# Optimization experiments

Hardware: AMD Instinct MI355X
Metric: run time of the kernel (lower is better)

Reference implementation:

```python
import jax, jax.numpy as jnp
import numpy as np

N_ITERS = 3
EPS = 1e-5


def _ln(x, g, b):
    mu = jnp.mean(x, axis=-1, keepdims=True)
    var = jnp.mean((x - mu) ** 2, axis=-1, keepdims=True)
    return (x - mu) * jax.lax.rsqrt(var + EPS) * g + b


def setup_inputs() -> dict:
    key = jax.random.key(0)
    ks = iter(jax.random.split(key, 32))
    B, N, D_in, H, K = 128, 1024, 192, 128, 3

    def lin(o, i):
        w = (jax.random.normal(next(ks), (o, i)) / np.sqrt(i)).astype(jnp.float32)
        return w, jnp.zeros((o,), jnp.float32)

    Wp, bp = lin(H, D_in)
    Wq, bq = lin(H, H)
    Wk, bk = lin(H, H)
    Wv, bv = lin(H, H)
    Wih, bih = lin(3 * H, H)   # GRUCell input weights, stacked [r, z, n]
    Whh, bhh = lin(3 * H, H)   # GRUCell hidden weights
    W1, b1 = lin(2 * H, H)     # MLP expand
    W2, b2 = lin(H, 2 * H)     # MLP project
    ones = jnp.ones((H,), jnp.float32)
    zeros = jnp.zeros((H,), jnp.float32)

    return {
        "patch_tokens": jax.random.normal(next(ks), (B, N, D_in), jnp.float32),
        "noise": jax.random.normal(next(ks), (B, K, H), jnp.float32),
        "slot_mu": (jax.random.normal(next(ks), (1, K, H)) * 0.02).astype(jnp.float32),
        "slot_log_sigma": jnp.zeros((1, K, H), jnp.float32),
        "Wp": Wp, "bp": bp, "g_in": ones, "b_in": zeros,
        "Wq": Wq, "bq": bq, "Wk": Wk, "bk": bk, "Wv": Wv, "bv": bv,
        "Wih": Wih, "bih": bih, "Whh": Whh, "bhh": bhh,
        "g_s": ones, "b_s": zeros,
        "W1": W1, "b1": b1, "W2": W2, "b2": b2,
        "g_m": ones, "b_m": zeros,
    }


def reference(patch_tokens, noise, slot_mu, slot_log_sigma,
              Wp, bp, g_in, b_in,
              Wq, bq, Wk, bk, Wv, bv,
              Wih, bih, Whh, bhh,
              g_s, b_s, W1, b1, W2, b2, g_m, b_m):
    H = slot_mu.shape[-1]
    scale = 1.0 / jnp.sqrt(jnp.asarray(H, patch_tokens.dtype))

    # project + LayerNorm inputs once (k, v depend only on inputs -> hoisted)
    inputs = _ln(patch_tokens @ Wp.T + bp, g_in, b_in)      # (B, N, H)
    k = inputs @ Wk.T + bk                                  # (B, N, H)
    v = inputs @ Wv.T + bv                                  # (B, N, H)

    slots = slot_mu + jnp.exp(slot_log_sigma) * noise       # (B, K, H)

    def gru_cell(x, h):
        gi = x @ Wih.T + bih                                # (B, K, 3H)
        gh = h @ Whh.T + bhh
        ir, iz, inn = jnp.split(gi, 3, axis=-1)
        hr, hz, hn = jnp.split(gh, 3, axis=-1)
        r = jax.nn.sigmoid(ir + hr)
        z = jax.nn.sigmoid(iz + hz)
        n = jnp.tanh(inn + r * hn)
        return (1.0 - z) * n + z * h

    attn_weights = None
    for _ in range(N_ITERS):
        slots_prev = slots
        s = _ln(slots, g_s, b_s)
        q = s @ Wq.T + bq                                   # (B, K, H)
        attn = jnp.einsum('bkd,bnd->bkn', q, k) * scale     # (B, K, N)
        attn_weights = jax.nn.softmax(attn, axis=1)         # softmax over slots
        updates = jnp.einsum('bkn,bnd->bkd', attn_weights, v)
        slots = gru_cell(updates, slots_prev)
        h = _ln(slots, g_m, b_m)
        slots = slots + (jax.nn.gelu(h @ W1.T + b1, approximate=False) @ W2.T + b2)

    return slots, attn_weights
```

## Files before the change

kernel.cpp:

```cpp
#include <hip/hip_runtime.h>
#include <math.h>

constexpr float EPS = 1e-5f;
constexpr float SCALE = 0.08838834764831845f;

using f32x4  = __attribute__((ext_vector_type(4))) float;
using bf16x8 = __attribute__((ext_vector_type(8))) short;
using us8    = __attribute__((ext_vector_type(8))) unsigned short;

__device__ __forceinline__ unsigned short f2b_rne(float f) {
    unsigned int x = __float_as_uint(f);
    return (unsigned short)((x + 0x7fffu + ((x >> 16) & 1u)) >> 16);
}

__device__ __forceinline__ int swz32(int row, int k8) {
    int f = (row & 3) ^ ((row >> 2) & 3);
    return row * 32 + ((k8 ^ f) << 3);
}

__global__ __launch_bounds__(256) void split_weights_kernel(
    const float* __restrict__ Wp, const float* __restrict__ Wk,
    const float* __restrict__ Wv, unsigned short* __restrict__ hi,
    unsigned short* __restrict__ lo)
{
    int idx = blockIdx.x * 256 + threadIdx.x;
    float v;
    if (idx < 24576)      v = Wp[idx];
    else if (idx < 40960) v = Wk[idx - 24576];
    else                  v = Wv[idx - 40960];
    unsigned int bits = __float_as_uint(v);
    hi[idx] = (unsigned short)(bits >> 16);
    lo[idx] = f2b_rne(v - __uint_as_float(bits & 0xffff0000u));
}

__global__ __launch_bounds__(256) void pack_weights_kernel(
    const float* __restrict__ Wih, const float* __restrict__ Whh,
    const float* __restrict__ W1, const float* __restrict__ W2,
    const float* __restrict__ Wq, float4* __restrict__ out)
{
    int idx = blockIdx.x * 256 + threadIdx.x;
    const float* src; int OUT, base, K;
    if (idx < 12288)      { src = Wih; OUT = 384; base = 0;     K = 128; }
    else if (idx < 24576) { src = Whh; OUT = 384; base = 12288; K = 128; }
    else if (idx < 32768) { src = W1;  OUT = 256; base = 24576; K = 128; }
    else if (idx < 40960) { src = W2;  OUT = 128; base = 32768; K = 256; }
    else                  { src = Wq;  OUT = 128; base = 40960; K = 128; }
    int li = idx - base;
    int kq = li / OUT, t = li - kq * OUT;
    float4 v;
    v.x = src[(size_t)t * K + 4 * kq];
    v.y = src[(size_t)t * K + 4 * kq + 1];
    v.z = src[(size_t)t * K + 4 * kq + 2];
    v.w = src[(size_t)t * K + 4 * kq + 3];
    out[idx] = v;
}

__global__ __launch_bounds__(256, 3) void fused_proj_kv_kernel(
    const float* __restrict__ patch,
    const unsigned short* __restrict__ Wphi, const unsigned short* __restrict__ Wplo,
    const unsigned short* __restrict__ Wkhi, const unsigned short* __restrict__ Wklo,
    const unsigned short* __restrict__ Wvhi, const unsigned short* __restrict__ Wvlo,
    const float* __restrict__ biasp, const float* __restrict__ g_in,
    const float* __restrict__ b_in, const float* __restrict__ biask,
    const float* __restrict__ biasv,
    float* __restrict__ kout, float* __restrict__ vout)
{
    __shared__ __align__(16) unsigned short mem[24576];

    const int tid  = threadIdx.x;
    const int lane = tid & 63, wave = tid >> 6;
    const int ln15 = lane & 15, quad = lane >> 4;
    const int m0   = blockIdx.x * 64;

    const int wrow = wave * 16;
    f32x4 acc1[8];
#pragma unroll
    for (int nt = 0; nt < 8; nt++)
#pragma unroll
        for (int r = 0; r < 4; r++) acc1[nt][r] = 0.f;

    const int arow = tid >> 2, ak8 = tid & 3;
    const float* aptr = patch + (size_t)(m0 + arow) * 192 + ak8 * 8;
    float4 pa0 = *(const float4*)aptr;
    float4 pa1 = *(const float4*)(aptr + 4);
    us8 pbh[2], pbl[2];
    int boff[2];
#pragma unroll
    for (int i = 0; i < 2; i++) {
        int c = tid + 256 * i;
        boff[i] = (c >> 2) * 192 + (c & 3) * 8;
        pbh[i] = *(const us8*)(Wphi + boff[i]);
        pbl[i] = *(const us8*)(Wplo + boff[i]);
    }

    const int ea = swz32(wrow + ln15, quad);

    for (int kk = 0; kk < 192; kk += 32) {
        {
            float va[8] = {pa0.x, pa0.y, pa0.z, pa0.w, pa1.x, pa1.y, pa1.z, pa1.w};
            us8 h, l;
#pragma unroll
            for (int j = 0; j < 8; j++) {
                unsigned int bits = __float_as_uint(va[j]);
                h[j] = (unsigned short)(bits >> 16);
                l[j] = f2b_rne(va[j] - __uint_as_float(bits & 0xffff0000u));
            }
            int e = swz32(arow, ak8);
            *(us8*)&mem[e]        = h;
            *(us8*)&mem[2048 + e] = l;
        }
#pragma unroll
        for (int i = 0; i < 2; i++) {
            int c = tid + 256 * i;
            int e = swz32(c >> 2, c & 3);
            *(us8*)&mem[4096 + e] = pbh[i];
            *(us8*)&mem[8192 + e] = pbl[i];
        }
        __syncthreads();

        int kn = kk + 32;
        if (kn < 192) {
            pa0 = *(const float4*)(aptr + kn);
            pa1 = *(const float4*)(aptr + kn + 4);
#pragma unroll
            for (int i = 0; i < 2; i++) {
                pbh[i] = *(const us8*)(Wphi + boff[i] + kn);
                pbl[i] = *(const us8*)(Wplo + boff[i] + kn);
            }
        }

        bf16x8 ah = *(const bf16x8*)&mem[ea];
        bf16x8 al = *(const bf16x8*)&mem[2048 + ea];
#pragma unroll
        for (int nt = 0; nt < 8; nt++) {
            int eb = swz32(nt * 16 + ln15, quad);
            bf16x8 bh = *(const bf16x8*)&mem[4096 + eb];
            bf16x8 bl = *(const bf16x8*)&mem[8192 + eb];
            acc1[nt] = __builtin_amdgcn_mfma_f32_16x16x32_bf16(ah, bh, acc1[nt], 0, 0, 0);
            acc1[nt] = __builtin_amdgcn_mfma_f32_16x16x32_bf16(ah, bl, acc1[nt], 0, 0, 0);
            acc1[nt] = __builtin_amdgcn_mfma_f32_16x16x32_bf16(al, bh, acc1[nt], 0, 0, 0);
        }
        __syncthreads();
    }

    us8 pw[4];
#pragma unroll
    for (int i = 0; i < 4; i++) {
        const unsigned short* pl = (i >> 1) ? Wklo : Wkhi;
        int c = tid + (i & 1) * 256;
        pw[i] = *(const us8*)(pl + (size_t)(c >> 2) * 128 + (c & 3) * 8);
    }

    {
        float bb[8], gg[8], be[8];
#pragma unroll
        for (int nt = 0; nt < 8; nt++) {
            int col = nt * 16 + ln15;
            bb[nt] = biasp[col]; gg[nt] = g_in[col]; be[nt] = b_in[col];
        }
#pragma unroll
        for (int nt = 0; nt < 8; nt++)
#pragma unroll
            for (int r = 0; r < 4; r++) acc1[nt][r] += bb[nt];

        float mu[4], rs[4];
#pragma unroll
        for (int r = 0; r < 4; r++) {
            float s = 0.f, s2 = 0.f;
#pragma unroll
            for (int nt = 0; nt < 8; nt++) {
                float v = acc1[nt][r];
                s += v; s2 += v * v;
            }
#pragma unroll
            for (int off = 1; off < 16; off <<= 1) {
                s  += __shfl_xor(s,  off, 64);
                s2 += __shfl_xor(s2, off, 64);
            }
            float m = s * (1.f / 128.f);
            mu[r] = m;
            rs[r] = rsqrtf(s2 * (1.f / 128.f) - m * m + EPS);
        }
#pragma unroll
        for (int nt = 0; nt < 8; nt++)
#pragma unroll
            for (int r = 0; r < 4; r++) {
                float v = (acc1[nt][r] - mu[r]) * rs[r] * gg[nt] + be[nt];
                int row = wrow + quad * 4 + r, col = nt * 16 + ln15;
                int xi = (row * 128 + col) ^ ((row & 7) << 3);
                unsigned int bits = __float_as_uint(v);
                mem[xi]        = (unsigned short)(bits >> 16);
                mem[8192 + xi] = f2b_rne(v - __uint_as_float(bits & 0xffff0000u));
            }
    }

    const int R  = (wave & 1) * 32;
    const int Cb = (wave >> 1) * 64;
    const int xorx = (ln15 & 7) << 3;

    float bbk[4], bbv[4];
#pragma unroll
    for (int nt = 0; nt < 4; nt++) {
        int col = Cb + nt * 16 + ln15;
        bbk[nt] = biask[col];
        bbv[nt] = biasv[col];
    }

    f32x4 acc[2][4];
#pragma unroll
    for (int mt = 0; mt < 2; mt++)
#pragma unroll
        for (int nt = 0; nt < 4; nt++)
#pragma unroll
            for (int r = 0; r < 4; r++) acc[mt][nt][r] = 0.f;

    for (int s = 0; s < 8; s++) {
#pragma unroll
        for (int i = 0; i < 4; i++) {
            int c = tid + (i & 1) * 256;
            int e = 16384 + (i >> 1) * 4096 + swz32(c >> 2, c & 3);
            *(us8*)&mem[e] = pw[i];
        }
        __syncthreads();

        if (s < 7) {
            int sn = s + 1, kkn = (sn & 3) * 32;
            const unsigned short* ph = (sn >> 2) ? Wvhi : Wkhi;
            const unsigned short* po = (sn >> 2) ? Wvlo : Wklo;
#pragma unroll
            for (int i = 0; i < 4; i++) {
                const unsigned short* pl = (i >> 1) ? po : ph;
                int c = tid + (i & 1) * 256;
                pw[i] = *(const us8*)(pl + (size_t)(c >> 2) * 128 + (c & 3) * 8 + kkn);
            }
        }

        int kk = (s & 3) * 32;
        bf16x8 xh[2], xl[2];
#pragma unroll
        for (int mt = 0; mt < 2; mt++) {
            int row = R + mt * 16 + ln15;
            int ei = (row * 128 + kk + quad * 8) ^ xorx;
            xh[mt] = *(const bf16x8*)&mem[ei];
            xl[mt] = *(const bf16x8*)&mem[8192 + ei];
        }
#pragma unroll
        for (int nt = 0; nt < 4; nt++) {
            int eb = 16384 + swz32(Cb + nt * 16 + ln15, quad);
            bf16x8 wh = *(const bf16x8*)&mem[eb];
            bf16x8 wl = *(const bf16x8*)&mem[4096 + eb];
#pragma unroll
            for (int mt = 0; mt < 2; mt++) {
                acc[mt][nt] = __builtin_amdgcn_mfma_f32_16x16x32_bf16(xh[mt], wh, acc[mt][nt], 0, 0, 0);
                acc[mt][nt] = __builtin_amdgcn_mfma_f32_16x16x32_bf16(xh[mt], wl, acc[mt][nt], 0, 0, 0);
                acc[mt][nt] = __builtin_amdgcn_mfma_f32_16x16x32_bf16(xl[mt], wh, acc[mt][nt], 0, 0, 0);
            }
        }

        if (s == 3) {
#pragma unroll
            for (int mt = 0; mt < 2; mt++)
#pragma unroll
                for (int nt = 0; nt < 4; nt++)
#pragma unroll
                    for (int r = 0; r < 4; r++) {
                        size_t o = (size_t)(m0 + R + mt * 16 + quad * 4 + r) * 128
                                 + Cb + nt * 16 + ln15;
                        kout[o] = acc[mt][nt][r] + bbk[nt];
                        acc[mt][nt][r] = 0.f;
                    }
        }
        if (s < 7) __syncthreads();
    }

#pragma unroll
    for (int mt = 0; mt < 2; mt++)
#pragma unroll
        for (int nt = 0; nt < 4; nt++)
#pragma unroll
            for (int r = 0; r < 4; r++) {
                size_t o = (size_t)(m0 + R + mt * 16 + quad * 4 + r) * 128
                         + Cb + nt * 16 + ln15;
                vout[o] = acc[mt][nt][r] + bbv[nt];
            }
}

__global__ __launch_bounds__(128) void init_lnq_kernel(
    const float* __restrict__ noise, const float* __restrict__ smu,
    const float* __restrict__ sls, const float* __restrict__ g_s,
    const float* __restrict__ b_s, const float4* __restrict__ WqT4,
    const float* __restrict__ bq, float* __restrict__ slots,
    float* __restrict__ q)
{
    __shared__ float s_l[128];
    __shared__ float red[4];
    const int row = blockIdx.x, tid = threadIdx.x;
    const int k = row % 3;
    float x = smu[k * 128 + tid] + expf(sls[k * 128 + tid]) * noise[row * 128 + tid];
    slots[row * 128 + tid] = x;

    float s = x, s2 = x * x;
#pragma unroll
    for (int off = 32; off >= 1; off >>= 1) {
        s += __shfl_down(s, off, 64); s2 += __shfl_down(s2, off, 64);
    }
    if ((tid & 63) == 0) { red[tid >> 6] = s; red[2 + (tid >> 6)] = s2; }
    __syncthreads();
    float S = red[0] + red[1], S2 = red[2] + red[3];
    float m = S * (1.f / 128.f);
    float r = rsqrtf(S2 * (1.f / 128.f) - m * m + EPS);
    s_l[tid] = (x - m) * r * g_s[tid] + b_s[tid];
    __syncthreads();

    float a = bq[tid];
#pragma unroll 8
    for (int kq = 0; kq < 32; kq++) {
        float4 w = WqT4[kq * 128 + tid];
        a += s_l[4 * kq] * w.x + s_l[4 * kq + 1] * w.y
           + s_l[4 * kq + 2] * w.z + s_l[4 * kq + 3] * w.w;
    }
    q[row * 128 + tid] = a;
}

__global__ __launch_bounds__(256) void attn_kernel(
    const float* __restrict__ q, const float* __restrict__ kbuf,
    const float* __restrict__ vbuf, float* __restrict__ upd_part,
    float* __restrict__ attn_out, int write_attn)
{
    __shared__ float q_l[3][132];
    __shared__ __align__(16) float kv[64][132];
    __shared__ float lg[3][64];
    __shared__ float w_l[3][64];
    const int b = blockIdx.y, chunk = blockIdx.x, n0 = chunk * 64, tid = threadIdx.x;

    for (int idx = tid; idx < 384; idx += 256) {
        int s = idx >> 7, c = idx & 127;
        q_l[s][c + (c >> 5)] = q[b * 384 + idx];
    }
    const float4* vg = (const float4*)(vbuf + ((size_t)b * 1024 + n0) * 128);
    for (int idx = tid; idx < 2048; idx += 256) {
        int n = idx >> 5, c = (idx & 31) * 4;
        *(float4*)&kv[n][c] = vg[idx];
    }
    const int n = tid >> 2, q4 = tid & 3;
    float4 kr[8];
    const float4* kg4 = (const float4*)(kbuf + ((size_t)b * 1024 + n0 + n) * 128 + q4 * 32);
#pragma unroll
    for (int i = 0; i < 8; i++) kr[i] = kg4[i];
    __syncthreads();

    {
        const float* q0 = &q_l[0][q4 * 33];
        const float* q1 = &q_l[1][q4 * 33];
        const float* q2 = &q_l[2][q4 * 33];
        float p0 = 0.f, p1 = 0.f, p2 = 0.f;
#pragma unroll
        for (int i = 0; i < 8; i++) {
            float kx[4] = {kr[i].x, kr[i].y, kr[i].z, kr[i].w};
#pragma unroll
            for (int j = 0; j < 4; j++) {
                float vv = kx[j];
                p0 += q0[4 * i + j] * vv;
                p1 += q1[4 * i + j] * vv;
                p2 += q2[4 * i + j] * vv;
            }
        }
        p0 += __shfl_xor(p0, 1, 64); p0 += __shfl_xor(p0, 2, 64);
        p1 += __shfl_xor(p1, 1, 64); p1 += __shfl_xor(p1, 2, 64);
        p2 += __shfl_xor(p2, 1, 64); p2 += __shfl_xor(p2, 2, 64);
        if (q4 == 0) {
            lg[0][n] = p0 * SCALE; lg[1][n] = p1 * SCALE; lg[2][n] = p2 * SCALE;
        }
    }
    __syncthreads();

    if (tid < 64) {
        float l0 = lg[0][tid], l1 = lg[1][tid], l2 = lg[2][tid];
        float m = fmaxf(l0, fmaxf(l1, l2));
        float e0 = expf(l0 - m), e1 = expf(l1 - m), e2 = expf(l2 - m);
        float inv = 1.f / (e0 + e1 + e2);
        w_l[0][tid] = e0 * inv; w_l[1][tid] = e1 * inv; w_l[2][tid] = e2 * inv;
        if (write_attn) {
            attn_out[b * 3072 + n0 + tid]        = e0 * inv;
            attn_out[b * 3072 + 1024 + n0 + tid] = e1 * inv;
            attn_out[b * 3072 + 2048 + n0 + tid] = e2 * inv;
        }
    }
    __syncthreads();

    if (tid < 128) {
        float p0 = 0.f, p1 = 0.f, p2 = 0.f;
#pragma unroll 8
        for (int nn = 0; nn < 64; nn++) {
            float vv = kv[nn][tid];
            p0 += w_l[0][nn] * vv; p1 += w_l[1][nn] * vv; p2 += w_l[2][nn] * vv;
        }
        size_t base = (((size_t)b * 16 + chunk) * 3) * 128 + tid;
        upd_part[base]       = p0;
        upd_part[base + 128] = p1;
        upd_part[base + 256] = p2;
    }
}

__global__ __launch_bounds__(384) void gru_mlp_kernel(
    const float* __restrict__ slots_in, const float* __restrict__ upd_part,
    const float4* __restrict__ WihT4, const float* __restrict__ bih,
    const float4* __restrict__ WhhT4, const float* __restrict__ bhh,
    const float* __restrict__ g_m, const float* __restrict__ b_m,
    const float4* __restrict__ W1T4, const float* __restrict__ b1,
    const float4* __restrict__ W2T4, const float* __restrict__ b2,
    const float* __restrict__ g_s, const float* __restrict__ b_s,
    const float4* __restrict__ WqT4, const float* __restrict__ bq,
    float* __restrict__ slots_out, float* __restrict__ q_out, int write_q)
{
    __shared__ float u2[2][128];
    __shared__ float u_l[128], h_l[128];
    __shared__ float r_l[128], z_l[128], in_l[128], hn_l[128];
    __shared__ float n_l[128], hid_l[256], w2p[256];
    __shared__ float red[4];
    const int row = blockIdx.x, tid = threadIdx.x;
    const int bb_ = row / 3, ss = row - bb_ * 3;

    if (tid < 256) {
        int col = tid & 127, half = tid >> 7;
        const float* up = upd_part + (((size_t)bb_ * 16 + half * 8) * 3 + ss) * 128 + col;
        float u = 0.f;
#pragma unroll
        for (int c = 0; c < 8; c++) u += up[(size_t)c * 384];
        u2[half][col] = u;
        if (half == 0) h_l[col] = slots_in[row * 128 + col];
    }
    __syncthreads();
    if (tid < 128) u_l[tid] = u2[0][tid] + u2[1][tid];
    __syncthreads();

    {
        float gi = bih[tid], gh = bhh[tid];
#pragma unroll 8
        for (int kq = 0; kq < 32; kq++) {
            float4 a = WihT4[kq * 384 + tid];
            float4 c = WhhT4[kq * 384 + tid];
            gi += u_l[4 * kq] * a.x + u_l[4 * kq + 1] * a.y
                + u_l[4 * kq + 2] * a.z + u_l[4 * kq + 3] * a.w;
            gh += h_l[4 * kq] * c.x + h_l[4 * kq + 1] * c.y
                + h_l[4 * kq + 2] * c.z + h_l[4 * kq + 3] * c.w;
        }
        if (tid < 128)      r_l[tid] = 1.f / (1.f + expf(-(gi + gh)));
        else if (tid < 256) z_l[tid - 128] = 1.f / (1.f + expf(-(gi + gh)));
        else { in_l[tid - 256] = gi; hn_l[tid - 256] = gh; }
    }
    __syncthreads();

    float hnew = 0.f;
    if (tid < 128) {
        float nn = tanhf(in_l[tid] + r_l[tid] * hn_l[tid]);
        hnew = (1.f - z_l[tid]) * nn + z_l[tid] * h_l[tid];
        float s = hnew, s2 = hnew * hnew;
#pragma unroll
        for (int off = 32; off >= 1; off >>= 1) {
            s += __shfl_down(s, off, 64); s2 += __shfl_down(s2, off, 64);
        }
        if ((tid & 63) == 0) { red[tid >> 6] = s; red[2 + (tid >> 6)] = s2; }
    }
    __syncthreads();
    if (tid < 128) {
        float S = red[0] + red[1], S2 = red[2] + red[3];
        float m1 = S * (1.f / 128.f);
        float r1 = rsqrtf(S2 * (1.f / 128.f) - m1 * m1 + EPS);
        n_l[tid] = (hnew - m1) * r1 * g_m[tid] + b_m[tid];
    }
    __syncthreads();

    if (tid < 256) {
        float a = b1[tid];
#pragma unroll 8
        for (int kq = 0; kq < 32; kq++) {
            float4 w = W1T4[kq * 256 + tid];
            a += n_l[4 * kq] * w.x + n_l[4 * kq + 1] * w.y
               + n_l[4 * kq + 2] * w.z + n_l[4 * kq + 3] * w.w;
        }
        a = 0.5f * a * (1.f + erff(a * 0.70710678118654752f));
        hid_l[tid] = a;
    }
    __syncthreads();

    if (tid < 256) {
        int out = tid & 127, half = tid >> 7;
        float p = 0.f;
#pragma unroll 8
        for (int kq = half * 32; kq < half * 32 + 32; kq++) {
            float4 w = W2T4[kq * 128 + out];
            p += hid_l[4 * kq] * w.x + hid_l[4 * kq + 1] * w.y
               + hid_l[4 * kq + 2] * w.z + hid_l[4 * kq + 3] * w.w;
        }
        w2p[tid] = p;
    }
    __syncthreads();

    float snew = 0.f;
    if (tid < 128) {
        snew = hnew + b2[tid] + (w2p[tid] + w2p[128 + tid]);
        slots_out[row * 128 + tid] = snew;
    }

    if (write_q) {
        if (tid < 128) {
            float t1 = snew, t2 = snew * snew;
#pragma unroll
            for (int off = 32; off >= 1; off >>= 1) {
                t1 += __shfl_down(t1, off, 64); t2 += __shfl_down(t2, off, 64);
            }
            if ((tid & 63) == 0) { red[tid >> 6] = t1; red[2 + (tid >> 6)] = t2; }
        }
        __syncthreads();
        if (tid < 128) {
            float T = red[0] + red[1], T2 = red[2] + red[3];
            float m2 = T * (1.f / 128.f);
            float r2 = rsqrtf(T2 * (1.f / 128.f) - m2 * m2 + EPS);
            n_l[tid] = (snew - m2) * r2 * g_s[tid] + b_s[tid];
        }
        __syncthreads();
        if (tid < 256) {
            int out = tid & 127, half = tid >> 7;
            float p = (half == 0) ? bq[out] : 0.f;
#pragma unroll 8
            for (int kq = half * 16; kq < half * 16 + 16; kq++) {
                float4 w = WqT4[kq * 128 + out];
                p += n_l[4 * kq] * w.x + n_l[4 * kq + 1] * w.y
                   + n_l[4 * kq + 2] * w.z + n_l[4 * kq + 3] * w.w;
            }
            w2p[tid] = p;
        }
        __syncthreads();
        if (tid < 128) q_out[row * 128 + tid] = w2p[tid] + w2p[128 + tid];
    }
}

extern "C" void kernel_launch(void* const* d_in, const int* in_sizes, int n_in,
                              void* d_out, int out_size, void* d_ws, size_t ws_size,
                              hipStream_t stream)
{
    const float* patch   = (const float*)d_in[0];
    const float* noise   = (const float*)d_in[1];
    const float* slot_mu = (const float*)d_in[2];
    const float* slot_ls = (const float*)d_in[3];
    const float* Wp = (const float*)d_in[4];  const float* bp = (const float*)d_in[5];
    const float* g_in = (const float*)d_in[6]; const float* b_in = (const float*)d_in[7];
    const float* Wq = (const float*)d_in[8];  const float* bq = (const float*)d_in[9];
    const float* Wk = (const float*)d_in[10]; const float* bk = (const float*)d_in[11];
    const float* Wv = (const float*)d_in[12]; const float* bv = (const float*)d_in[13];
    const float* Wih = (const float*)d_in[14]; const float* bih = (const float*)d_in[15];
    const float* Whh = (const float*)d_in[16]; const float* bhh = (const float*)d_in[17];
    const float* g_s = (const float*)d_in[18]; const float* b_s = (const float*)d_in[19];
    const float* W1 = (const float*)d_in[20]; const float* b1 = (const float*)d_in[21];
    const float* W2 = (const float*)d_in[22]; const float* b2 = (const float*)d_in[23];
    const float* g_m = (const float*)d_in[24]; const float* b_m = (const float*)d_in[25];

    float* kbuf = (float*)d_ws;
    float* vbuf = kbuf + 16777216;
    unsigned short* w_hi = (unsigned short*)(vbuf + 16777216);
    unsigned short* w_lo = w_hi + 57344;
    unsigned short* wp_hi = w_hi,        * wp_lo = w_lo;
    unsigned short* wk_hi = w_hi + 24576,* wk_lo = w_lo + 24576;
    unsigned short* wv_hi = w_hi + 40960,* wv_lo = w_lo + 40960;
    float4* wt4 = (float4*)(w_lo + 57344);
    float4* wihT4 = wt4;
    float4* whhT4 = wt4 + 12288;
    float4* w1T4  = wt4 + 24576;
    float4* w2T4  = wt4 + 32768;
    float4* wqT4  = wt4 + 40960;
    float* slots = (float*)(wt4 + 45056);
    float* qbuf  = slots + 49152;
    float* part  = qbuf + 49152;

    float* out_slots = (float*)d_out;
    float* out_attn  = (float*)d_out + 49152;

    split_weights_kernel<<<224, 256, 0, stream>>>(Wp, Wk, Wv, w_hi, w_lo);
    pack_weights_kernel<<<176, 256, 0, stream>>>(Wih, Whh, W1, W2, Wq, wt4);

    fused_proj_kv_kernel<<<2048, 256, 0, stream>>>(
        patch, wp_hi, wp_lo, wk_hi, wk_lo, wv_hi, wv_lo,
        bp, g_in, b_in, bk, bv, kbuf, vbuf);

    init_lnq_kernel<<<384, 128, 0, stream>>>(noise, slot_mu, slot_ls,
                                             g_s, b_s, wqT4, bq, slots, qbuf);

    for (int it = 0; it < 3; it++) {
        attn_kernel<<<dim3(16, 128), 256, 0, stream>>>(
            qbuf, kbuf, vbuf, part, out_attn, it == 2 ? 1 : 0);
        gru_mlp_kernel<<<384, 384, 0, stream>>>(
            slots, part, wihT4, bih, whhT4, bhh, g_m, b_m, w1T4, b1, w2T4, b2,
            g_s, b_s, wqT4, bq,
            (it == 2) ? out_slots : slots, qbuf, it == 2 ? 0 : 1);
    }
}
```

Before: 379.5 us.

## Read GEMM weights from global directly, restructure attention chunks, merge weight prep

The projection and K/V GEMMs stop staging weight tiles in shared memory. Each wave now reads the bf16 hi/lo weight fragments straight from global/L2 memory, and K and V are computed in one pass with separate accumulators, which removes per-step barriers. The attention kernel handles 128-token chunks and keeps V in registers, with a shared-memory partial reduction replacing the shared K/V tile. The number of partial update chunks drops from 16 to 8, and the two weight-prep kernels are merged into one launch. The cost is more register pressure and repeated uncoalesced global weight reads that rely on cache hits.

```diff
diff --git a/kernel.cpp b/kernel.cpp
--- a/kernel.cpp
+++ b/kernel.cpp
@@ -13,46 +13,40 @@
     return (unsigned short)((x + 0x7fffu + ((x >> 16) & 1u)) >> 16);
 }
 
-__device__ __forceinline__ int swz32(int row, int k8) {
-    int f = (row & 3) ^ ((row >> 2) & 3);
-    return row * 32 + ((k8 ^ f) << 3);
-}
-
-__global__ __launch_bounds__(256) void split_weights_kernel(
+__global__ __launch_bounds__(256) void prep_weights_kernel(
     const float* __restrict__ Wp, const float* __restrict__ Wk,
-    const float* __restrict__ Wv, unsigned short* __restrict__ hi,
-    unsigned short* __restrict__ lo)
+    const float* __restrict__ Wv, const float* __restrict__ Wih,
+    const float* __restrict__ Whh, const float* __restrict__ W1,
+    const float* __restrict__ W2, const float* __restrict__ Wq,
+    unsigned short* __restrict__ hi, unsigned short* __restrict__ lo,
+    float4* __restrict__ wt4)
 {
     int idx = blockIdx.x * 256 + threadIdx.x;
-    float v;
-    if (idx < 24576)      v = Wp[idx];
-    else if (idx < 40960) v = Wk[idx - 24576];
-    else                  v = Wv[idx - 40960];
-    unsigned int bits = __float_as_uint(v);
-    hi[idx] = (unsigned short)(bits >> 16);
-    lo[idx] = f2b_rne(v - __uint_as_float(bits & 0xffff0000u));
-}
-
-__global__ __launch_bounds__(256) void pack_weights_kernel(
-    const float* __restrict__ Wih, const float* __restrict__ Whh,
-    const float* __restrict__ W1, const float* __restrict__ W2,
-    const float* __restrict__ Wq, float4* __restrict__ out)
-{
-    int idx = blockIdx.x * 256 + threadIdx.x;
-    const float* src; int OUT, base, K;
-    if (idx < 12288)      { src = Wih; OUT = 384; base = 0;     K = 128; }
-    else if (idx < 24576) { src = Whh; OUT = 384; base = 12288; K = 128; }
-    else if (idx < 32768) { src = W1;  OUT = 256; base = 24576; K = 128; }
-    else if (idx < 40960) { src = W2;  OUT = 128; base = 32768; K = 256; }
-    else                  { src = Wq;  OUT = 128; base = 40960; K = 128; }
-    int li = idx - base;
-    int kq = li / OUT, t = li - kq * OUT;
-    float4 v;
-    v.x = src[(size_t)t * K + 4 * kq];
-    v.y = src[(size_t)t * K + 4 * kq + 1];
-    v.z = src[(size_t)t * K + 4 * kq + 2];
-    v.w = src[(size_t)t * K + 4 * kq + 3];
-    out[idx] = v;
+    if (idx < 57344) {
+        float v;
+        if (idx < 24576)      v = Wp[idx];
+        else if (idx < 40960) v = Wk[idx - 24576];
+        else                  v = Wv[idx - 40960];
+        unsigned int bits = __float_as_uint(v);
+        hi[idx] = (unsigned short)(bits >> 16);
+        lo[idx] = f2b_rne(v - __uint_as_float(bits & 0xffff0000u));
+    } else {
+        int li = idx - 57344;
+        const float* src; int OUT, base, K;
+        if (li < 12288)      { src = Wih; OUT = 384; base = 0;     K = 128; }
+        else if (li < 24576) { src = Whh; OUT = 384; base = 12288; K = 128; }
+        else if (li < 32768) { src = W1;  OUT = 256; base = 24576; K = 128; }
+        else if (li < 40960) { src = W2;  OUT = 128; base = 32768; K = 256; }
+        else                 { src = Wq;  OUT = 128; base = 40960; K = 128; }
+        int lo2 = li - base;
+        int kq = lo2 / OUT, t = lo2 - kq * OUT;
+        float4 v;
+        v.x = src[(size_t)t * K + 4 * kq];
+        v.y = src[(size_t)t * K + 4 * kq + 1];
+        v.z = src[(size_t)t * K + 4 * kq + 2];
+        v.w = src[(size_t)t * K + 4 * kq + 3];
+        wt4[li] = v;
+    }
 }
 
 __global__ __launch_bounds__(256, 3) void fused_proj_kv_kernel(
@@ -71,33 +65,28 @@
     const int lane = tid & 63, wave = tid >> 6;
     const int ln15 = lane & 15, quad = lane >> 4;
     const int m0   = blockIdx.x * 64;
-
     const int wrow = wave * 16;
+
     f32x4 acc1[8];
 #pragma unroll
     for (int nt = 0; nt < 8; nt++)
 #pragma unroll
         for (int r = 0; r < 4; r++) acc1[nt][r] = 0.f;
 
-    const int arow = tid >> 2, ak8 = tid & 3;
-    const float* aptr = patch + (size_t)(m0 + arow) * 192 + ak8 * 8;
-    float4 pa0 = *(const float4*)aptr;
-    float4 pa1 = *(const float4*)(aptr + 4);
-    us8 pbh[2], pbl[2];
-    int boff[2];
-#pragma unroll
-    for (int i = 0; i < 2; i++) {
-        int c = tid + 256 * i;
-        boff[i] = (c >> 2) * 192 + (c & 3) * 8;
-        pbh[i] = *(const us8*)(Wphi + boff[i]);
-        pbl[i] = *(const us8*)(Wplo + boff[i]);
-    }
-
-    const int ea = swz32(wrow + ln15, quad);
-
-    for (int kk = 0; kk < 192; kk += 32) {
-        {
-            float va[8] = {pa0.x, pa0.y, pa0.z, pa0.w, pa1.x, pa1.y, pa1.z, pa1.w};
+    const int ar0 = tid >> 3, ak8 = tid & 7;
+    const float* ap0 = patch + (size_t)(m0 + ar0) * 192 + ak8 * 8;
+    const float* ap1 = patch + (size_t)(m0 + ar0 + 32) * 192 + ak8 * 8;
+
+    float4 pa[2][2];
+    pa[0][0] = *(const float4*)ap0; pa[0][1] = *(const float4*)(ap0 + 4);
+    pa[1][0] = *(const float4*)ap1; pa[1][1] = *(const float4*)(ap1 + 4);
+
+#pragma unroll
+    for (int ss = 0; ss < 3; ss++) {
+#pragma unroll
+        for (int i = 0; i < 2; i++) {
+            float va[8] = {pa[i][0].x, pa[i][0].y, pa[i][0].z, pa[i][0].w,
+                           pa[i][1].x, pa[i][1].y, pa[i][1].z, pa[i][1].w};
             us8 h, l;
 #pragma unroll
             for (int j = 0; j < 8; j++) {
@@ -105,50 +94,38 @@
                 h[j] = (unsigned short)(bits >> 16);
                 l[j] = f2b_rne(va[j] - __uint_as_float(bits & 0xffff0000u));
             }
-            int e = swz32(arow, ak8);
-            *(us8*)&mem[e]        = h;
-            *(us8*)&mem[2048 + e] = l;
-        }
-#pragma unroll
-        for (int i = 0; i < 2; i++) {
-            int c = tid + 256 * i;
-            int e = swz32(c >> 2, c & 3);
-            *(us8*)&mem[4096 + e] = pbh[i];
-            *(us8*)&mem[8192 + e] = pbl[i];
+            int row = ar0 + i * 32;
+            int e = row * 64 + ((ak8 ^ (row & 7)) << 3);
+            *(us8*)&mem[16384 + e] = h;
+            *(us8*)&mem[20480 + e] = l;
         }
         __syncthreads();
 
-        int kn = kk + 32;
-        if (kn < 192) {
-            pa0 = *(const float4*)(aptr + kn);
-            pa1 = *(const float4*)(aptr + kn + 4);
-#pragma unroll
-            for (int i = 0; i < 2; i++) {
-                pbh[i] = *(const us8*)(Wphi + boff[i] + kn);
-                pbl[i] = *(const us8*)(Wplo + boff[i] + kn);
-            }
-        }
-
-        bf16x8 ah = *(const bf16x8*)&mem[ea];
-        bf16x8 al = *(const bf16x8*)&mem[2048 + ea];
-#pragma unroll
-        for (int nt = 0; nt < 8; nt++) {
-            int eb = swz32(nt * 16 + ln15, quad);
-            bf16x8 bh = *(const bf16x8*)&mem[4096 + eb];
-            bf16x8 bl = *(const bf16x8*)&mem[8192 + eb];
-            acc1[nt] = __builtin_amdgcn_mfma_f32_16x16x32_bf16(ah, bh, acc1[nt], 0, 0, 0);
-            acc1[nt] = __builtin_amdgcn_mfma_f32_16x16x32_bf16(ah, bl, acc1[nt], 0, 0, 0);
-            acc1[nt] = __builtin_amdgcn_mfma_f32_16x16x32_bf16(al, bh, acc1[nt], 0, 0, 0);
+        if (ss < 2) {
+            int kn = (ss + 1) * 64;
+            pa[0][0] = *(const float4*)(ap0 + kn); pa[0][1] = *(const float4*)(ap0 + kn + 4);
+            pa[1][0] = *(const float4*)(ap1 + kn); pa[1][1] = *(const float4*)(ap1 + kn + 4);
+        }
+
+#pragma unroll
+        for (int kh = 0; kh < 2; kh++) {
+            int row = wrow + ln15;
+            int k8q = kh * 4 + quad;
+            int ea = row * 64 + ((k8q ^ (row & 7)) << 3);
+            bf16x8 ah = *(const bf16x8*)&mem[16384 + ea];
+            bf16x8 al = *(const bf16x8*)&mem[20480 + ea];
+            int kgl = ss * 64 + kh * 32 + quad * 8;
+#pragma unroll
+            for (int nt = 0; nt < 8; nt++) {
+                size_t wo = (size_t)(nt * 16 + ln15) * 192 + kgl;
+                bf16x8 bh = *(const bf16x8*)(Wphi + wo);
+                bf16x8 bl = *(const bf16x8*)(Wplo + wo);
+                acc1[nt] = __builtin_amdgcn_mfma_f32_16x16x32_bf16(ah, bh, acc1[nt], 0, 0, 0);
+                acc1[nt] = __builtin_amdgcn_mfma_f32_16x16x32_bf16(ah, bl, acc1[nt], 0, 0, 0);
+                acc1[nt] = __builtin_amdgcn_mfma_f32_16x16x32_bf16(al, bh, acc1[nt], 0, 0, 0);
+            }
         }
         __syncthreads();
-    }
-
-    us8 pw[4];
-#pragma unroll
-    for (int i = 0; i < 4; i++) {
-        const unsigned short* pl = (i >> 1) ? Wklo : Wkhi;
-        int c = tid + (i & 1) * 256;
-        pw[i] = *(const us8*)(pl + (size_t)(c >> 2) * 128 + (c & 3) * 8);
     }
 
     {
@@ -193,96 +170,48 @@
                 mem[8192 + xi] = f2b_rne(v - __uint_as_float(bits & 0xffff0000u));
             }
     }
-
-    const int R  = (wave & 1) * 32;
-    const int Cb = (wave >> 1) * 64;
-    const int xorx = (ln15 & 7) << 3;
-
-    float bbk[4], bbv[4];
-#pragma unroll
-    for (int nt = 0; nt < 4; nt++) {
-        int col = Cb + nt * 16 + ln15;
-        bbk[nt] = biask[col];
-        bbv[nt] = biasv[col];
-    }
-
-    f32x4 acc[2][4];
-#pragma unroll
-    for (int mt = 0; mt < 2; mt++)
-#pragma unroll
-        for (int nt = 0; nt < 4; nt++)
-#pragma unroll
-            for (int r = 0; r < 4; r++) acc[mt][nt][r] = 0.f;
-
-    for (int s = 0; s < 8; s++) {
-#pragma unroll
-        for (int i = 0; i < 4; i++) {
-            int c = tid + (i & 1) * 256;
-            int e = 16384 + (i >> 1) * 4096 + swz32(c >> 2, c & 3);
-            *(us8*)&mem[e] = pw[i];
-        }
-        __syncthreads();
-
-        if (s < 7) {
-            int sn = s + 1, kkn = (sn & 3) * 32;
-            const unsigned short* ph = (sn >> 2) ? Wvhi : Wkhi;
-            const unsigned short* po = (sn >> 2) ? Wvlo : Wklo;
-#pragma unroll
-            for (int i = 0; i < 4; i++) {
-                const unsigned short* pl = (i >> 1) ? po : ph;
-                int c = tid + (i & 1) * 256;
-                pw[i] = *(const us8*)(pl + (size_t)(c >> 2) * 128 + (c & 3) * 8 + kkn);
-            }
-        }
-
-        int kk = (s & 3) * 32;
-        bf16x8 xh[2], xl[2];
-#pragma unroll
-        for (int mt = 0; mt < 2; mt++) {
-            int row = R + mt * 16 + ln15;
-            int ei = (row * 128 + kk + quad * 8) ^ xorx;
-            xh[mt] = *(const bf16x8*)&mem[ei];
-            xl[mt] = *(const bf16x8*)&mem[8192 + ei];
-        }
-#pragma unroll
-        for (int nt = 0; nt < 4; nt++) {
-            int eb = 16384 + swz32(Cb + nt * 16 + ln15, quad);
-            bf16x8 wh = *(const bf16x8*)&mem[eb];
-            bf16x8 wl = *(const bf16x8*)&mem[4096 + eb];
-#pragma unroll
-            for (int mt = 0; mt < 2; mt++) {
-                acc[mt][nt] = __builtin_amdgcn_mfma_f32_16x16x32_bf16(xh[mt], wh, acc[mt][nt], 0, 0, 0);
-                acc[mt][nt] = __builtin_amdgcn_mfma_f32_16x16x32_bf16(xh[mt], wl, acc[mt][nt], 0, 0, 0);
-                acc[mt][nt] = __builtin_amdgcn_mfma_f32_16x16x32_bf16(xl[mt], wh, acc[mt][nt], 0, 0, 0);
-            }
-        }
-
-        if (s == 3) {
-#pragma unroll
-            for (int mt = 0; mt < 2; mt++)
-#pragma unroll
-                for (int nt = 0; nt < 4; nt++)
-#pragma unroll
-                    for (int r = 0; r < 4; r++) {
-                        size_t o = (size_t)(m0 + R + mt * 16 + quad * 4 + r) * 128
-                                 + Cb + nt * 16 + ln15;
-                        kout[o] = acc[mt][nt][r] + bbk[nt];
-                        acc[mt][nt][r] = 0.f;
-                    }
-        }
-        if (s < 7) __syncthreads();
-    }
-
-#pragma unroll
-    for (int mt = 0; mt < 2; mt++)
-#pragma unroll
-        for (int nt = 0; nt < 4; nt++)
-#pragma unroll
-            for (int r = 0; r < 4; r++) {
-                size_t o = (size_t)(m0 + R + mt * 16 + quad * 4 + r) * 128
-                         + Cb + nt * 16 + ln15;
-                vout[o] = acc[mt][nt][r] + bbv[nt];
-            }
+    __syncthreads();
+
+    f32x4 acck[8], accv[8];
+#pragma unroll
+    for (int nt = 0; nt < 8; nt++)
+#pragma unroll
+        for (int r = 0; r < 4; r++) { acck[nt][r] = 0.f; accv[nt][r] = 0.f; }
+
+#pragma unroll
+    for (int ks = 0; ks < 4; ks++) {
+        int kk = ks * 32;
+        int row = wrow + ln15;
+        int ei = (row * 128 + kk + quad * 8) ^ ((row & 7) << 3);
+        bf16x8 xh = *(const bf16x8*)&mem[ei];
+        bf16x8 xl = *(const bf16x8*)&mem[8192 + ei];
+#pragma unroll
+        for (int nt = 0; nt < 8; nt++) {
+            size_t wo = (size_t)(nt * 16 + ln15) * 128 + kk + quad * 8;
+            bf16x8 wkh = *(const bf16x8*)(Wkhi + wo);
+            bf16x8 wkl = *(const bf16x8*)(Wklo + wo);
+            bf16x8 wvh = *(const bf16x8*)(Wvhi + wo);
+            bf16x8 wvl = *(const bf16x8*)(Wvlo + wo);
+            acck[nt] = __builtin_amdgcn_mfma_f32_16x16x32_bf16(xh, wkh, acck[nt], 0, 0, 0);
+            acck[nt] = __builtin_amdgcn_mfma_f32_16x16x32_bf16(xh, wkl, acck[nt], 0, 0, 0);
+            acck[nt] = __builtin_amdgcn_mfma_f32_16x16x32_bf16(xl, wkh, acck[nt], 0, 0, 0);
+            accv[nt] = __builtin_amdgcn_mfma_f32_16x16x32_bf16(xh, wvh, accv[nt], 0, 0, 0);
+            accv[nt] = __builtin_amdgcn_mfma_f32_16x16x32_bf16(xh, wvl, accv[nt], 0, 0, 0);
+            accv[nt] = __builtin_amdgcn_mfma_f32_16x16x32_bf16(xl, wvh, accv[nt], 0, 0, 0);
+        }
+    }
+
+#pragma unroll
+    for (int nt = 0; nt < 8; nt++) {
+        int col = nt * 16 + ln15;
+        float bk_ = biask[col], bv_ = biasv[col];
+#pragma unroll
+        for (int r = 0; r < 4; r++) {
+            size_t o = (size_t)(m0 + wrow + quad * 4 + r) * 128 + col;
+            kout[o] = acck[nt][r] + bk_;
+            vout[o] = accv[nt][r] + bv_;
+        }
+    }
 }
 
 __global__ __launch_bounds__(128) void init_lnq_kernel(
@@ -322,83 +251,100 @@
     q[row * 128 + tid] = a;
 }
 
-__global__ __launch_bounds__(256) void attn_kernel(
+__global__ __launch_bounds__(256, 3) void attn_kernel(
     const float* __restrict__ q, const float* __restrict__ kbuf,
     const float* __restrict__ vbuf, float* __restrict__ upd_part,
     float* __restrict__ attn_out, int write_attn)
 {
     __shared__ float q_l[3][132];
-    __shared__ __align__(16) float kv[64][132];
-    __shared__ float lg[3][64];
-    __shared__ float w_l[3][64];
-    const int b = blockIdx.y, chunk = blockIdx.x, n0 = chunk * 64, tid = threadIdx.x;
+    __shared__ float lg[3][128];
+    __shared__ float w_l[3][128];
+    __shared__ float part[8][3][128];
+    const int b = blockIdx.y, chunk = blockIdx.x, n0 = chunk * 128, tid = threadIdx.x;
 
     for (int idx = tid; idx < 384; idx += 256) {
         int s = idx >> 7, c = idx & 127;
         q_l[s][c + (c >> 5)] = q[b * 384 + idx];
     }
-    const float4* vg = (const float4*)(vbuf + ((size_t)b * 1024 + n0) * 128);
-    for (int idx = tid; idx < 2048; idx += 256) {
-        int n = idx >> 5, c = (idx & 31) * 4;
-        *(float4*)&kv[n][c] = vg[idx];
-    }
-    const int n = tid >> 2, q4 = tid & 3;
-    float4 kr[8];
-    const float4* kg4 = (const float4*)(kbuf + ((size_t)b * 1024 + n0 + n) * 128 + q4 * 32);
-#pragma unroll
-    for (int i = 0; i < 8; i++) kr[i] = kg4[i];
+
+    const int tg = tid >> 5, d0 = (tid & 31) * 4;
+    const float* vp = vbuf + ((size_t)b * 1024 + n0 + tg * 16) * 128 + d0;
+    float4 vreg[16];
+#pragma unroll
+    for (int j = 0; j < 16; j++) vreg[j] = *(const float4*)(vp + (size_t)j * 128);
+
     __syncthreads();
 
     {
-        const float* q0 = &q_l[0][q4 * 33];
-        const float* q1 = &q_l[1][q4 * 33];
-        const float* q2 = &q_l[2][q4 * 33];
+        const int n = tid >> 1, h = tid & 1;
+        const float4* kp = (const float4*)(kbuf + ((size_t)b * 1024 + n0 + n) * 128 + h * 64);
         float p0 = 0.f, p1 = 0.f, p2 = 0.f;
 #pragma unroll
-        for (int i = 0; i < 8; i++) {
-            float kx[4] = {kr[i].x, kr[i].y, kr[i].z, kr[i].w};
-#pragma unroll
-            for (int j = 0; j < 4; j++) {
-                float vv = kx[j];
-                p0 += q0[4 * i + j] * vv;
-                p1 += q1[4 * i + j] * vv;
-                p2 += q2[4 * i + j] * vv;
-            }
-        }
-        p0 += __shfl_xor(p0, 1, 64); p0 += __shfl_xor(p0, 2, 64);
-        p1 += __shfl_xor(p1, 1, 64); p1 += __shfl_xor(p1, 2, 64);
-        p2 += __shfl_xor(p2, 1, 64); p2 += __shfl_xor(p2, 2, 64);
-        if (q4 == 0) {
+        for (int jj = 0; jj < 2; jj++) {
+            const float* q0 = &q_l[0][h * 66 + jj * 33];
+            const float* q1 = &q_l[1][h * 66 + jj * 33];
+            const float* q2 = &q_l[2][h * 66 + jj * 33];
+#pragma unroll
+            for (int f = 0; f < 8; f++) {
+                float4 kk4 = kp[jj * 8 + f];
+                float kx[4] = {kk4.x, kk4.y, kk4.z, kk4.w};
+#pragma unroll
+                for (int e = 0; e < 4; e++) {
+                    float vv = kx[e];
+                    p0 += q0[f * 4 + e] * vv;
+                    p1 += q1[f * 4 + e] * vv;
+                    p2 += q2[f * 4 + e] * vv;
+                }
+            }
+        }
+        p0 += __shfl_xor(p0, 1, 64);
+        p1 += __shfl_xor(p1, 1, 64);
+        p2 += __shfl_xor(p2, 1, 64);
+        if (h == 0) {
             lg[0][n] = p0 * SCALE; lg[1][n] = p1 * SCALE; lg[2][n] = p2 * SCALE;
         }
     }
     __syncthreads();
 
-    if (tid < 64) {
+    if (tid < 128) {
         float l0 = lg[0][tid], l1 = lg[1][tid], l2 = lg[2][tid];
         float m = fmaxf(l0, fmaxf(l1, l2));
         float e0 = expf(l0 - m), e1 = expf(l1 - m), e2 = expf(l2 - m);
         float inv = 1.f / (e0 + e1 + e2);
         w_l[0][tid] = e0 * inv; w_l[1][tid] = e1 * inv; w_l[2][tid] = e2 * inv;
         if (write_attn) {
-            attn_out[b * 3072 + n0 + tid]        = e0 * inv;
-            attn_out[b * 3072 + 1024 + n0 + tid] = e1 * inv;
-            attn_out[b * 3072 + 2048 + n0 + tid] = e2 * inv;
-        }
-    }
-    __syncthreads();
-
-    if (tid < 128) {
-        float p0 = 0.f, p1 = 0.f, p2 = 0.f;
-#pragma unroll 8
-        for (int nn = 0; nn < 64; nn++) {
-            float vv = kv[nn][tid];
-            p0 += w_l[0][nn] * vv; p1 += w_l[1][nn] * vv; p2 += w_l[2][nn] * vv;
-        }
-        size_t base = (((size_t)b * 16 + chunk) * 3) * 128 + tid;
-        upd_part[base]       = p0;
-        upd_part[base + 128] = p1;
-        upd_part[base + 256] = p2;
+            int n = n0 + tid;
+            attn_out[b * 3072 + n]        = e0 * inv;
+            attn_out[b * 3072 + 1024 + n] = e1 * inv;
+            attn_out[b * 3072 + 2048 + n] = e2 * inv;
+        }
+    }
+    __syncthreads();
+
+    {
+        float4 a0 = {0.f, 0.f, 0.f, 0.f}, a1 = a0, a2 = a0;
+#pragma unroll
+        for (int j = 0; j < 16; j++) {
+            float w0 = w_l[0][tg * 16 + j];
+            float w1 = w_l[1][tg * 16 + j];
+            float w2 = w_l[2][tg * 16 + j];
+            float4 vv = vreg[j];
+            a0.x += w0 * vv.x; a0.y += w0 * vv.y; a0.z += w0 * vv.z; a0.w += w0 * vv.w;
+            a1.x += w1 * vv.x; a1.y += w1 * vv.y; a1.z += w1 * vv.z; a1.w += w1 * vv.w;
+            a2.x += w2 * vv.x; a2.y += w2 * vv.y; a2.z += w2 * vv.z; a2.w += w2 * vv.w;
+        }
+        *(float4*)&part[tg][0][d0] = a0;
+        *(float4*)&part[tg][1][d0] = a1;
+        *(float4*)&part[tg][2][d0] = a2;
+    }
+    __syncthreads();
+
+    for (int idx = tid; idx < 384; idx += 256) {
+        int s = idx >> 7, d = idx & 127;
+        float u = 0.f;
+#pragma unroll
+        for (int g = 0; g < 8; g++) u += part[g][s][d];
+        upd_part[(((size_t)b * 8 + chunk) * 3 + s) * 128 + d] = u;
     }
 }
 
@@ -423,10 +369,10 @@
 
     if (tid < 256) {
         int col = tid & 127, half = tid >> 7;
-        const float* up = upd_part + (((size_t)bb_ * 16 + half * 8) * 3 + ss) * 128 + col;
+        const float* up = upd_part + (((size_t)bb_ * 8 + half * 4) * 3 + ss) * 128 + col;
         float u = 0.f;
 #pragma unroll
-        for (int c = 0; c < 8; c++) u += up[(size_t)c * 384];
+        for (int c = 0; c < 4; c++) u += up[(size_t)c * 384];
         u2[half][col] = u;
         if (half == 0) h_l[col] = slots_in[row * 128 + col];
     }
@@ -576,8 +522,8 @@
     float* out_slots = (float*)d_out;
     float* out_attn  = (float*)d_out + 49152;
 
-    split_weights_kernel<<<224, 256, 0, stream>>>(Wp, Wk, Wv, w_hi, w_lo);
-    pack_weights_kernel<<<176, 256, 0, stream>>>(Wih, Whh, W1, W2, Wq, wt4);
+    prep_weights_kernel<<<400, 256, 0, stream>>>(
+        Wp, Wk, Wv, Wih, Whh, W1, W2, Wq, w_hi, w_lo, wt4);
 
     fused_proj_kv_kernel<<<2048, 256, 0, stream>>>(
         patch, wp_hi, wp_lo, wk_hi, wk_lo, wv_hi, wv_lo,
@@ -587,7 +533,7 @@
                                              g_s, b_s, wqT4, bq, slots, qbuf);
 
     for (int it = 0; it < 3; it++) {
-        attn_kernel<<<dim3(16, 128), 256, 0, stream>>>(
+        attn_kernel<<<dim3(8, 128), 256, 0, stream>>>(
             qbuf, kbuf, vbuf, part, out_attn, it == 2 ? 1 : 0);
         gru_mlp_kernel<<<384, 384, 0, stream>>>(
             slots, part, wihT4, bih, whhT4, bhh, g_m, b_m, w1T4, b1, w2T4, b2,
```

Result: slower. 560.4 us (+47.7%).

## Merge weight prep kernels, remap proj blocks, preload patch rows, register-stage V in attention

Applied to the files above, without the earlier changes.

The two weight preparation kernels become one launch to save a kernel launch. The projection kernel remaps block indices, loads all six 32-wide K slices of the patch row into registers up front, and fully unrolls its inner loops. The attention kernel keeps V in registers instead of shared memory, so all 256 threads compute partial weighted sums that are then reduced through shared memory. These changes aim to cut launch overhead and memory latency and to use all threads in the update sum, at the cost of higher register pressure.

```diff
diff --git a/kernel.cpp b/kernel.cpp
--- a/kernel.cpp
+++ b/kernel.cpp
@@ -18,41 +18,40 @@
     return row * 32 + ((k8 ^ f) << 3);
 }
 
-__global__ __launch_bounds__(256) void split_weights_kernel(
+__global__ __launch_bounds__(256) void prep_weights_kernel(
     const float* __restrict__ Wp, const float* __restrict__ Wk,
-    const float* __restrict__ Wv, unsigned short* __restrict__ hi,
-    unsigned short* __restrict__ lo)
+    const float* __restrict__ Wv, const float* __restrict__ Wih,
+    const float* __restrict__ Whh, const float* __restrict__ W1,
+    const float* __restrict__ W2, const float* __restrict__ Wq,
+    unsigned short* __restrict__ hi, unsigned short* __restrict__ lo,
+    float4* __restrict__ wt4)
 {
     int idx = blockIdx.x * 256 + threadIdx.x;
-    float v;
-    if (idx < 24576)      v = Wp[idx];
-    else if (idx < 40960) v = Wk[idx - 24576];
-    else                  v = Wv[idx - 40960];
-    unsigned int bits = __float_as_uint(v);
-    hi[idx] = (unsigned short)(bits >> 16);
-    lo[idx] = f2b_rne(v - __uint_as_float(bits & 0xffff0000u));
-}
-
-__global__ __launch_bounds__(256) void pack_weights_kernel(
-    const float* __restrict__ Wih, const float* __restrict__ Whh,
-    const float* __restrict__ W1, const float* __restrict__ W2,
-    const float* __restrict__ Wq, float4* __restrict__ out)
-{
-    int idx = blockIdx.x * 256 + threadIdx.x;
-    const float* src; int OUT, base, K;
-    if (idx < 12288)      { src = Wih; OUT = 384; base = 0;     K = 128; }
-    else if (idx < 24576) { src = Whh; OUT = 384; base = 12288; K = 128; }
-    else if (idx < 32768) { src = W1;  OUT = 256; base = 24576; K = 128; }
-    else if (idx < 40960) { src = W2;  OUT = 128; base = 32768; K = 256; }
-    else                  { src = Wq;  OUT = 128; base = 40960; K = 128; }
-    int li = idx - base;
-    int kq = li / OUT, t = li - kq * OUT;
-    float4 v;
-    v.x = src[(size_t)t * K + 4 * kq];
-    v.y = src[(size_t)t * K + 4 * kq + 1];
-    v.z = src[(size_t)t * K + 4 * kq + 2];
-    v.w = src[(size_t)t * K + 4 * kq + 3];
-    out[idx] = v;
+    if (idx < 57344) {
+        float v;
+        if (idx < 24576)      v = Wp[idx];
+        else if (idx < 40960) v = Wk[idx - 24576];
+        else                  v = Wv[idx - 40960];
+        unsigned int bits = __float_as_uint(v);
+        hi[idx] = (unsigned short)(bits >> 16);
+        lo[idx] = f2b_rne(v - __uint_as_float(bits & 0xffff0000u));
+    } else {
+        int li = idx - 57344;
+        const float* src; int OUT, base, K;
+        if (li < 12288)      { src = Wih; OUT = 384; base = 0;     K = 128; }
+        else if (li < 24576) { src = Whh; OUT = 384; base = 12288; K = 128; }
+        else if (li < 32768) { src = W1;  OUT = 256; base = 24576; K = 128; }
+        else if (li < 40960) { src = W2;  OUT = 128; base = 32768; K = 256; }
+        else                 { src = Wq;  OUT = 128; base = 40960; K = 128; }
+        int lo2 = li - base;
+        int kq = lo2 / OUT, t = lo2 - kq * OUT;
+        float4 v;
+        v.x = src[(size_t)t * K + 4 * kq];
+        v.y = src[(size_t)t * K + 4 * kq + 1];
+        v.z = src[(size_t)t * K + 4 * kq + 2];
+        v.w = src[(size_t)t * K + 4 * kq + 3];
+        wt4[li] = v;
+    }
 }
 
 __global__ __launch_bounds__(256, 3) void fused_proj_kv_kernel(
@@ -70,7 +69,8 @@
     const int tid  = threadIdx.x;
     const int lane = tid & 63, wave = tid >> 6;
     const int ln15 = lane & 15, quad = lane >> 4;
-    const int m0   = blockIdx.x * 64;
+    const int bid  = blockIdx.x;
+    const int m0   = ((bid & 7) * 256 + (bid >> 3)) * 64;
 
     const int wrow = wave * 16;
     f32x4 acc1[8];
@@ -81,8 +81,12 @@
 
     const int arow = tid >> 2, ak8 = tid & 3;
     const float* aptr = patch + (size_t)(m0 + arow) * 192 + ak8 * 8;
-    float4 pa0 = *(const float4*)aptr;
-    float4 pa1 = *(const float4*)(aptr + 4);
+    float4 pa[6][2];
+#pragma unroll
+    for (int t6 = 0; t6 < 6; t6++) {
+        pa[t6][0] = *(const float4*)(aptr + t6 * 32);
+        pa[t6][1] = *(const float4*)(aptr + t6 * 32 + 4);
+    }
     us8 pbh[2], pbl[2];
     int boff[2];
 #pragma unroll
@@ -95,9 +99,11 @@
 
     const int ea = swz32(wrow + ln15, quad);
 
-    for (int kk = 0; kk < 192; kk += 32) {
+#pragma unroll
+    for (int st = 0; st < 6; st++) {
         {
-            float va[8] = {pa0.x, pa0.y, pa0.z, pa0.w, pa1.x, pa1.y, pa1.z, pa1.w};
+            float va[8] = {pa[st][0].x, pa[st][0].y, pa[st][0].z, pa[st][0].w,
+                           pa[st][1].x, pa[st][1].y, pa[st][1].z, pa[st][1].w};
             us8 h, l;
 #pragma unroll
             for (int j = 0; j < 8; j++) {
@@ -118,10 +124,8 @@
         }
         __syncthreads();
 
-        int kn = kk + 32;
-        if (kn < 192) {
-            pa0 = *(const float4*)(aptr + kn);
-            pa1 = *(const float4*)(aptr + kn + 4);
+        if (st < 5) {
+            int kn = (st + 1) * 32;
 #pragma unroll
             for (int i = 0; i < 2; i++) {
                 pbh[i] = *(const us8*)(Wphi + boff[i] + kn);
@@ -214,6 +218,7 @@
 #pragma unroll
             for (int r = 0; r < 4; r++) acc[mt][nt][r] = 0.f;
 
+#pragma unroll
     for (int s = 0; s < 8; s++) {
 #pragma unroll
         for (int i = 0; i < 4; i++) {
@@ -328,20 +333,22 @@
     float* __restrict__ attn_out, int write_attn)
 {
     __shared__ float q_l[3][132];
-    __shared__ __align__(16) float kv[64][132];
     __shared__ float lg[3][64];
     __shared__ float w_l[3][64];
+    __shared__ float part[8][3][128];
     const int b = blockIdx.y, chunk = blockIdx.x, n0 = chunk * 64, tid = threadIdx.x;
 
     for (int idx = tid; idx < 384; idx += 256) {
         int s = idx >> 7, c = idx & 127;
         q_l[s][c + (c >> 5)] = q[b * 384 + idx];
     }
-    const float4* vg = (const float4*)(vbuf + ((size_t)b * 1024 + n0) * 128);
-    for (int idx = tid; idx < 2048; idx += 256) {
-        int n = idx >> 5, c = (idx & 31) * 4;
-        *(float4*)&kv[n][c] = vg[idx];
-    }
+
+    const int tg = tid >> 5, d0 = (tid & 31) * 4;
+    const float* vp = vbuf + ((size_t)b * 1024 + n0 + tg * 8) * 128 + d0;
+    float4 vreg[8];
+#pragma unroll
+    for (int j = 0; j < 8; j++) vreg[j] = *(const float4*)(vp + (size_t)j * 128);
+
     const int n = tid >> 2, q4 = tid & 3;
     float4 kr[8];
     const float4* kg4 = (const float4*)(kbuf + ((size_t)b * 1024 + n0 + n) * 128 + q4 * 32);
@@ -388,17 +395,30 @@
     }
     __syncthreads();
 
-    if (tid < 128) {
-        float p0 = 0.f, p1 = 0.f, p2 = 0.f;
-#pragma unroll 8
-        for (int nn = 0; nn < 64; nn++) {
-            float vv = kv[nn][tid];
-            p0 += w_l[0][nn] * vv; p1 += w_l[1][nn] * vv; p2 += w_l[2][nn] * vv;
-        }
-        size_t base = (((size_t)b * 16 + chunk) * 3) * 128 + tid;
-        upd_part[base]       = p0;
-        upd_part[base + 128] = p1;
-        upd_part[base + 256] = p2;
+    {
+        float4 a0 = {0.f, 0.f, 0.f, 0.f}, a1 = a0, a2 = a0;
+#pragma unroll
+        for (int j = 0; j < 8; j++) {
+            float w0 = w_l[0][tg * 8 + j];
+            float w1 = w_l[1][tg * 8 + j];
+            float w2 = w_l[2][tg * 8 + j];
+            float4 vv = vreg[j];
+            a0.x += w0 * vv.x; a0.y += w0 * vv.y; a0.z += w0 * vv.z; a0.w += w0 * vv.w;
+            a1.x += w1 * vv.x; a1.y += w1 * vv.y; a1.z += w1 * vv.z; a1.w += w1 * vv.w;
+            a2.x += w2 * vv.x; a2.y += w2 * vv.y; a2.z += w2 * vv.z; a2.w += w2 * vv.w;
+        }
+        *(float4*)&part[tg][0][d0] = a0;
+        *(float4*)&part[tg][1][d0] = a1;
+        *(float4*)&part[tg][2][d0] = a2;
+    }
+    __syncthreads();
+
+    for (int idx = tid; idx < 384; idx += 256) {
+        int s = idx >> 7, d = idx & 127;
+        float u = 0.f;
+#pragma unroll
+        for (int g = 0; g < 8; g++) u += part[g][s][d];
+        upd_part[(((size_t)b * 16 + chunk) * 3 + s) * 128 + d] = u;
     }
 }
 
@@ -576,8 +596,8 @@
     float* out_slots = (float*)d_out;
     float* out_attn  = (float*)d_out + 49152;
 
-    split_weights_kernel<<<224, 256, 0, stream>>>(Wp, Wk, Wv, w_hi, w_lo);
-    pack_weights_kernel<<<176, 256, 0, stream>>>(Wih, Whh, W1, W2, Wq, wt4);
+    prep_weights_kernel<<<400, 256, 0, stream>>>(
+        Wp, Wk, Wv, Wih, Whh, W1, W2, Wq, w_hi, w_lo, wt4);
 
     fused_proj_kv_kernel<<<2048, 256, 0, stream>>>(
         patch, wp_hi, wp_lo, wk_hi, wk_lo, wv_hi, wv_lo,
```

Result: faster. 365.2 us (-3.7%).
